# Kernel optimization log

Measured on AMD Instinct MI355X. Metric: run time of the kernel, lower is better.

## Reference

```python
import jax, jax.numpy as jnp
import numpy as np

RPN_BBOX_STD_DEV = np.array([0.1, 0.1, 0.2, 0.2], dtype=np.float32)
PRE_NMS_LIMIT = 6000
PROPOSAL_COUNT = 1000
NMS_THRESHOLD = 0.7
BATCH = 8
NUM_ANCHORS = 261888


def setup_inputs() -> dict:
    key = jax.random.key(0)
    k1, k2, k3, k4 = jax.random.split(key, 4)
    fg = jax.random.uniform(k1, (BATCH, NUM_ANCHORS), dtype=jnp.float32)
    rpn_probs = jnp.stack([1.0 - fg, fg], axis=-1)  # [B, N, 2] (bg, fg)
    rpn_bbox = jax.random.normal(k2, (BATCH, NUM_ANCHORS, 4), dtype=jnp.float32) * 0.5
    # valid normalized anchors: y_min < y_max, x_min < x_max, inside [0, 1]
    mins = jax.random.uniform(k3, (BATCH, NUM_ANCHORS, 2), minval=0.0, maxval=0.85)
    size = jax.random.uniform(k4, (BATCH, NUM_ANCHORS, 2), minval=0.02, maxval=0.15)
    anchors = jnp.concatenate([mins, mins + size], axis=-1)  # [B, N, 4]
    return {"rpn_probs": rpn_probs, "rpn_bbox": rpn_bbox, "anchors": anchors}


def apply_box_deltas(boxes, deltas):
    # boxes: [..., (y1, x1, y2, x2)], deltas: [..., (dy, dx, log(dh), log(dw))]
    h = boxes[..., 2] - boxes[..., 0]
    w = boxes[..., 3] - boxes[..., 1]
    cy = boxes[..., 0] + 0.5 * h + deltas[..., 0] * h
    cx = boxes[..., 1] + 0.5 * w + deltas[..., 1] * w
    h = h * jnp.exp(deltas[..., 2])
    w = w * jnp.exp(deltas[..., 3])
    y1 = cy - 0.5 * h
    x1 = cx - 0.5 * w
    return jnp.stack([y1, x1, y1 + h, x1 + w], axis=-1)


def pairwise_iou(boxes):
    # boxes: [N, 4] -> iou [N, N]
    y1, x1, y2, x2 = boxes[:, 0], boxes[:, 1], boxes[:, 2], boxes[:, 3]
    area = (y2 - y1) * (x2 - x1)
    ih = jnp.maximum(jnp.minimum(y2[:, None], y2[None, :]) - jnp.maximum(y1[:, None], y1[None, :]), 0.0)
    iw = jnp.maximum(jnp.minimum(x2[:, None], x2[None, :]) - jnp.maximum(x1[:, None], x1[None, :]), 0.0)
    inter = ih * iw
    union = area[:, None] + area[None, :] - inter
    return jnp.where(union > 0.0, inter / union, 0.0)


def nms_single(boxes):
    # boxes: [K, 4], already sorted by score descending (top_k sorted=True).
    # Greedy NMS: a box is suppressed if it overlaps (IoU > thresh) a kept,
    # higher-scoring box. Sequential suppression via lax.scan over rows.
    K = boxes.shape[0]
    iou = pairwise_iou(boxes)  # [K, K]
    order = jnp.arange(K)

    def step(keep, i):
        suppress = keep[i] & (iou[i] > NMS_THRESHOLD) & (order > i)
        return keep & ~suppress, None

    keep, _ = jax.lax.scan(step, jnp.ones((K,), dtype=bool), order)
    # gather kept boxes in score order, pad with zeros to PROPOSAL_COUNT
    rank = jnp.cumsum(keep) - 1
    valid = keep & (rank < PROPOSAL_COUNT)
    dest = jnp.where(valid, rank, PROPOSAL_COUNT)  # invalid rows -> scratch row
    out = jnp.zeros((PROPOSAL_COUNT + 1, 4), boxes.dtype).at[dest].set(boxes)
    return out[:PROPOSAL_COUNT]


def reference(rpn_probs, rpn_bbox, anchors):
    scores = rpn_probs[:, :, 1]  # fg prob [B, N]
    deltas = rpn_bbox * jnp.asarray(RPN_BBOX_STD_DEV).reshape(1, 1, 4)
    k = min(PRE_NMS_LIMIT, anchors.shape[1])
    top_scores, idx = jax.lax.top_k(scores, k)  # sorted descending, [B, K]
    deltas_k = jnp.take_along_axis(deltas, idx[..., None], axis=1)   # [B, K, 4]
    anchors_k = jnp.take_along_axis(anchors, idx[..., None], axis=1)  # [B, K, 4]
    boxes = jnp.clip(apply_box_deltas(anchors_k, deltas_k), 0.0, 1.0)
    proposals = jax.vmap(nms_single)(boxes)  # [B, PROPOSAL_COUNT, 4]
    return proposals
```

## Files before the change

### kernel.cpp

```cpp
#include <hip/hip_runtime.h>
#include <hip/hip_bf16.h>

typedef unsigned long long ull;

constexpr int BATCH = 8;
constexpr int NA    = 261888;
constexpr int KSEL  = 6000;
constexpr int PROP  = 1000;
constexpr int CAP   = 8192;
constexpr int NBINS = 8192;
constexpr int HB    = 16;
constexpr int NB    = (KSEL + 63) / 64;
constexpr int NWP   = 94;
constexpr int NBLK  = 94;
constexpr int NBLK2 = 47;

constexpr size_t OFF_CNT   = 0;
constexpr size_t OFF_TSEL  = 512;
constexpr size_t OFF_BOXES = 544;
constexpr size_t OFF_MASK  = 769024;
constexpr size_t OFF_DIAG  = OFF_MASK + 36096000;
constexpr size_t OFF_SUP   = OFF_DIAG + 385024;
constexpr size_t OFF_KEYS  = OFF_MASK;
constexpr size_t OFF_RANK  = OFF_MASK + 524288;
constexpr size_t OFF_HIST  = OFF_MASK + 2097152;

__device__ __forceinline__ int score_bin(float s) {
  int b = (int)(s * (float)NBINS);
  if (b < 0) b = 0;
  if (b > NBINS - 1) b = NBINS - 1;
  return b;
}

__global__ __launch_bounds__(256) void hist_kernel(const float2* __restrict__ probs,
                                                   unsigned int* __restrict__ hist) {
  __shared__ unsigned int lh[NBINS];
  for (int i = threadIdx.x; i < NBINS; i += 256) lh[i] = 0u;
  __syncthreads();
  int b = blockIdx.y;
  const float2* p = probs + (size_t)b * NA;
  for (int a = blockIdx.x * 256 + threadIdx.x; a < NA; a += HB * 256) {
    atomicAdd(&lh[score_bin(p[a].y)], 1u);
  }
  __syncthreads();
  unsigned int* gh = hist + ((size_t)b * HB + blockIdx.x) * NBINS;
  for (int i = threadIdx.x; i < NBINS; i += 256) gh[i] = lh[i];
}

__global__ __launch_bounds__(256) void thresh_kernel(const unsigned int* __restrict__ hist,
                                                     int* __restrict__ tsel) {
  constexpr int GR = NBINS / 256;
  __shared__ unsigned int ch[NBINS];
  __shared__ unsigned int gsum[256];
  int b = blockIdx.x;
  const unsigned int* h = hist + (size_t)b * HB * NBINS;
  for (int bin = threadIdx.x; bin < NBINS; bin += 256) {
    unsigned int s = 0;
    for (int k = 0; k < HB; ++k) s += h[(size_t)k * NBINS + bin];
    ch[bin] = s;
  }
  __syncthreads();
  unsigned int s = 0;
  int g0 = threadIdx.x * GR;
  for (int i = 0; i < GR; ++i) s += ch[g0 + i];
  gsum[threadIdx.x] = s;
  __syncthreads();
  if (threadIdx.x == 0) {
    unsigned int acc = 0;
    int g = 255;
    for (; g > 0; --g) {
      if (acc + gsum[g] >= (unsigned)KSEL) break;
      acc += gsum[g];
    }
    int t = g * GR;
    for (int bin = g * GR + GR - 1; bin >= g * GR; --bin) {
      acc += ch[bin];
      if (acc >= (unsigned)KSEL) { t = bin; break; }
    }
    tsel[b] = t;
  }
}

__global__ __launch_bounds__(256) void compact_kernel(const float2* __restrict__ probs,
                                                      const int* __restrict__ tsel,
                                                      int* __restrict__ cnt,
                                                      ull* __restrict__ keys) {
  __shared__ int lcnt, lbase;
  __shared__ ull lbuf[2048];
  int b = blockIdx.y;
  int t = tsel[b];
  if (threadIdx.x == 0) lcnt = 0;
  __syncthreads();
  const float2* p = probs + (size_t)b * NA;
  for (int a = blockIdx.x * blockDim.x + threadIdx.x; a < NA; a += gridDim.x * blockDim.x) {
    float s = p[a].y;
    if (score_bin(s) >= t) {
      int pos = atomicAdd(&lcnt, 1);
      unsigned int ib = ~__float_as_uint(s);
      lbuf[pos] = ((ull)ib << 32) | (unsigned int)a;
    }
  }
  __syncthreads();
  if (threadIdx.x == 0) lbase = atomicAdd(&cnt[b * 16], lcnt);
  __syncthreads();
  int n = lcnt, base = lbase;
  ull* kb = keys + (size_t)b * CAP;
  for (int i = threadIdx.x; i < n; i += 256) {
    int pos = base + i;
    if (pos < CAP) kb[pos] = lbuf[i];
  }
}

__global__ __launch_bounds__(256) void rank_kernel(const int* __restrict__ cnt,
                                                   const ull* __restrict__ keys,
                                                   unsigned int* __restrict__ rank) {
  int b = blockIdx.z;
  int n = cnt[b * 16];
  if (n > CAP) n = CAP;
  int i = blockIdx.x * 256 + threadIdx.x;
  if (i >= n) return;
  const ull* kb = keys + (size_t)b * CAP;
  ull my = kb[i];
  int n16 = (n + 15) & ~15;
  int nchunks = n16 >> 4;
  int hc = nchunks >> 1;
  int jlo = (blockIdx.y == 0) ? 0 : hc * 16;
  int jhi = (blockIdx.y == 0) ? hc * 16 : n16;
  unsigned int r = 0;
  for (int j = jlo; j < jhi; j += 16) {
#pragma unroll
    for (int t = 0; t < 16; ++t) {
      r += (kb[j + t] < my) ? 1u : 0u;
    }
  }
  if (r) atomicAdd(&rank[(size_t)b * CAP + i], r);
}

__global__ __launch_bounds__(256) void scatter_kernel(const float4* __restrict__ anchors4,
                                                      const float4* __restrict__ bbox4,
                                                      const int* __restrict__ cnt,
                                                      const ull* __restrict__ keys,
                                                      const unsigned int* __restrict__ rank,
                                                      float4* __restrict__ boxes4) {
#pragma clang fp contract(off)
  int b = blockIdx.y;
  int n = cnt[b * 16];
  if (n > CAP) n = CAP;
  int i = blockIdx.x * 256 + threadIdx.x;
  if (i >= n) return;
  unsigned int r = rank[(size_t)b * CAP + i];
  if (r >= (unsigned)KSEL) return;
  int a = (int)(unsigned int)(keys[(size_t)b * CAP + i] & 0xffffffffull);
  float4 anc = anchors4[(size_t)b * NA + a];
  float4 d   = bbox4[(size_t)b * NA + a];
  float h = anc.z - anc.x;
  float w = anc.w - anc.y;
  float dy = d.x * 0.1f, dx = d.y * 0.1f, dh = d.z * 0.2f, dw = d.w * 0.2f;
  float cy = (anc.x + (0.5f * h)) + (dy * h);
  float cx = (anc.y + (0.5f * w)) + (dx * w);
  float h2 = h * expf(dh);
  float w2 = w * expf(dw);
  float y1 = cy - 0.5f * h2;
  float x1 = cx - 0.5f * w2;
  float y2 = y1 + h2;
  float x2 = x1 + w2;
  y1 = fminf(fmaxf(y1, 0.f), 1.f);
  x1 = fminf(fmaxf(x1, 0.f), 1.f);
  y2 = fminf(fmaxf(y2, 0.f), 1.f);
  x2 = fminf(fmaxf(x2, 0.f), 1.f);
  boxes4[(size_t)b * KSEL + r] = make_float4(y1, x1, y2, x2);
}

__global__ __launch_bounds__(256) void mask_kernel(const float4* __restrict__ boxes4,
                                                   ull* __restrict__ mask,
                                                   ull* __restrict__ diagT,
                                                   ull* __restrict__ superT) {
#pragma clang fp contract(off)
  int cx = blockIdx.x, rb2 = blockIdx.y, b = blockIdx.z;
  int w0 = 2 * rb2;
  int cb0 = w0 + 4 * cx;
  if (cb0 >= NWP) return;
  __shared__ float4 colbox[4][64];
  __shared__ float  colca[4][64];
  __shared__ ull wtile[128][5];
  int tid = threadIdx.x, wv = tid >> 6, l = tid & 63;
  int cb = cb0 + wv;
  int rA = rb2 * 128 + l, rB = rA + 64;
  float4 zero = make_float4(0.f, 0.f, 0.f, 0.f);
  float4 boxA = (rA < KSEL) ? boxes4[(size_t)b * KSEL + rA] : zero;
  float4 boxB = (rB < KSEL) ? boxes4[(size_t)b * KSEL + rB] : zero;
  float areaA = (boxA.z - boxA.x) * (boxA.w - boxA.y);
  float areaB = (boxB.z - boxB.x) * (boxB.w - boxB.y);
  int c = cb * 64 + l;
  float4 cload = (cb < NB && c < KSEL) ? boxes4[(size_t)b * KSEL + c] : zero;
  colbox[wv][l] = cload;
  colca[wv][l] = (cload.z - cload.x) * (cload.w - cload.y);
  __syncthreads();
  ull bitsA = 0ull, bitsB = 0ull;
  if (cb < NB) {
#pragma unroll
    for (int u = 0; u < 64; ++u) {
      float4 cbx = colbox[wv][u];
      float ca = colca[wv][u];
      {
        float ih = fmaxf(fminf(boxA.z, cbx.z) - fmaxf(boxA.x, cbx.x), 0.f);
        float iw = fmaxf(fminf(boxA.w, cbx.w) - fmaxf(boxA.y, cbx.y), 0.f);
        float inter = ih * iw;
        float uni = (areaA + ca) - inter;
        float d = fmaf(-0.7f, uni, inter);
        float tt = 6e-7f * uni;
        bool keep;
        if (__builtin_fabsf(d) <= tt) keep = (inter / uni) > 0.7f;
        else keep = d > 0.f;
        if (keep) bitsA |= (1ull << u);
      }
      {
        float ih = fmaxf(fminf(boxB.z, cbx.z) - fmaxf(boxB.x, cbx.x), 0.f);
        float iw = fmaxf(fminf(boxB.w, cbx.w) - fmaxf(boxB.y, cbx.y), 0.f);
        float inter = ih * iw;
        float uni = (areaB + ca) - inter;
        float d = fmaf(-0.7f, uni, inter);
        float tt = 6e-7f * uni;
        bool keep;
        if (__builtin_fabsf(d) <= tt) keep = (inter / uni) > 0.7f;
        else keep = d > 0.f;
        if (keep) bitsB |= (1ull << u);
      }
    }
    if (cb == w0) {
      bitsA &= (l == 63) ? 0ull : (~0ull << (l + 1));
      ull colT = 0ull;
#pragma unroll
      for (int k = 0; k < 64; ++k) {
        ull bk = __ballot(((bitsA >> k) & 1ull) != 0ull);
        if (l == k) colT = bk;
      }
      diagT[((size_t)b * NBLK + w0) * 64 + l] = colT;
    }
    if (cb == w0 + 1) {
      superT[((size_t)b * NBLK + w0) * 64 + l] = bitsA;
      bitsB &= (l == 63) ? 0ull : (~0ull << (l + 1));
      ull colT = 0ull;
#pragma unroll
      for (int k = 0; k < 64; ++k) {
        ull bk = __ballot(((bitsB >> k) & 1ull) != 0ull);
        if (l == k) colT = bk;
      }
      diagT[((size_t)b * NBLK + w0 + 1) * 64 + l] = colT;
    }
    if (cb == w0 + 2) {
      superT[((size_t)b * NBLK + w0 + 1) * 64 + l] = bitsB;
    }
  }
  wtile[l][wv] = bitsA;
  wtile[l + 64][wv] = bitsB;
  __syncthreads();
  int base_row = rb2 * 128;
#pragma unroll
  for (int pass = 0; pass < 2; ++pass) {
    int idx = pass * 256 + tid;
    int rr = idx >> 2, w = idx & 3;
    int row = base_row + rr;
    if (row < KSEL && cb0 + w < NWP)
      mask[((size_t)b * KSEL + row) * NWP + cb0 + w] = wtile[rr][w];
  }
}

__global__ __launch_bounds__(256, 1) void scan_kernel(const float4* __restrict__ boxes4,
                                                      const ull* __restrict__ mask,
                                                      const ull* __restrict__ diagT,
                                                      const ull* __restrict__ superT,
                                                      float4* __restrict__ out4) {
  __shared__ ull ldiagT[NBLK * 64];
  __shared__ ull lsuper[NBLK * 64];
  __shared__ ull S[96];
  __shared__ ull S_urg;
  __shared__ int klist[2][64];
  __shared__ int skeep[1024];
  __shared__ int s_kept, s_done, s_klen[2];
  int b = blockIdx.x;
  int tid = threadIdx.x;
  int lane = tid & 63;
  const ull* mb = mask + (size_t)b * KSEL * NWP;

  const ull* dt = diagT + (size_t)b * NBLK * 64;
  const ull* st = superT + (size_t)b * NBLK * 64;
  for (int i = tid; i < NBLK * 64; i += 256) { ldiagT[i] = dt[i]; lsuper[i] = st[i]; }
  if (tid < 96) S[tid] = 0ull;
  if (tid == 0) { s_kept = 0; s_done = 0; s_klen[0] = 0; s_klen[1] = 0; S_urg = 0ull; }
  __syncthreads();

  for (int n = 0; n < NBLK; ++n) {
    if (tid < 64) {
      ull Sn = S[n] | S_urg;
      int i0 = n * 64;
      ull colT = ldiagT[i0 + lane];
      ull sd = (n + 1 < NBLK) ? lsuper[i0 + lane] : 0ull;
      int nval = KSEL - i0;
      ull valid = (nval >= 64) ? ~0ull : ((1ull << nval) - 1ull);
      ull A = ~Sn & valid;
      ull K = 0ull;
      int kept = s_kept;
      int done = 0;
      while (A) {
        int u = __builtin_ctzll(A);
        ++kept;
        K |= (1ull << u);
        if (kept >= PROP) { done = 1; break; }
        ull sup = __ballot(((colT >> u) & 1ull) != 0ull);
        A &= ~(sup | (1ull << u));
      }
      int klen = __builtin_popcountll(K);
      int kbase = kept - klen;
      if ((K >> lane) & 1ull) {
        int rank = __builtin_popcountll(K & ((1ull << lane) - 1ull));
        skeep[kbase + rank] = i0 + lane;
        klist[n & 1][rank] = i0 + lane;
      }
      int klp = (klen + 7) & ~7;
      if (klen > 0 && lane >= klen && lane < klp)
        klist[n & 1][lane] = i0 + __builtin_ctzll(K);
      unsigned ulo = (unsigned)sd, uhi = (unsigned)(sd >> 32);
      if (!((K >> lane) & 1ull)) { ulo = 0u; uhi = 0u; }
#pragma unroll
      for (int m = 1; m < 64; m <<= 1) {
        ulo |= (unsigned)__shfl_xor((int)ulo, m, 64);
        uhi |= (unsigned)__shfl_xor((int)uhi, m, 64);
      }
      if (lane == 0) {
        s_klen[n & 1] = klen;
        S_urg = (ull)ulo | ((ull)uhi << 32);
        s_kept = kept;
        if (done || n == NBLK - 1) s_done = 1;
      }
    } else {
      int prev = (n & 1) ^ 1;
      int kl = s_klen[prev];
      int w = n + 1 + (tid - 64);
      if (kl > 0 && w < NB) {
        const int* kp = klist[prev];
        ull acc = 0ull;
        int klp = (kl + 7) & ~7;
        for (int ri = 0; ri < klp; ri += 8) {
#pragma unroll
          for (int t2 = 0; t2 < 8; ++t2)
            acc |= mb[(size_t)kp[ri + t2] * NWP + w];
        }
        S[w] |= acc;
      }
    }
    __syncthreads();
    if (s_done) break;
  }

  int fin = s_kept;
  if (fin > PROP) fin = PROP;
  for (int r2 = tid; r2 < PROP; r2 += 256) {
    float4 v = make_float4(0.f, 0.f, 0.f, 0.f);
    if (r2 < fin) v = boxes4[(size_t)b * KSEL + skeep[r2]];
    out4[(size_t)b * PROP + r2] = v;
  }
}

extern "C" void kernel_launch(void* const* d_in, const int* in_sizes, int n_in,
                              void* d_out, int out_size, void* d_ws, size_t ws_size,
                              hipStream_t stream) {
  const float2* probs   = (const float2*)d_in[0];
  const float4* bbox4   = (const float4*)d_in[1];
  const float4* anchors4= (const float4*)d_in[2];
  float4* out4 = (float4*)d_out;
  char* ws = (char*)d_ws;

  int* cnt           = (int*)(ws + OFF_CNT);
  int* tsel          = (int*)(ws + OFF_TSEL);
  float4* boxes4     = (float4*)(ws + OFF_BOXES);
  ull* maskw         = (ull*)(ws + OFF_MASK);
  ull* diagT         = (ull*)(ws + OFF_DIAG);
  ull* superT        = (ull*)(ws + OFF_SUP);
  ull* keys          = (ull*)(ws + OFF_KEYS);
  unsigned int* rank = (unsigned int*)(ws + OFF_RANK);
  unsigned int* hist = (unsigned int*)(ws + OFF_HIST);

  hipMemsetAsync(ws + OFF_CNT, 0, 544, stream);
  hipMemsetAsync(ws + OFF_KEYS, 0xFF, 524288, stream);
  hipMemsetAsync(ws + OFF_RANK, 0, 262144, stream);

  hipLaunchKernelGGL(hist_kernel,    dim3(HB, BATCH),      dim3(256), 0, stream, probs, hist);
  hipLaunchKernelGGL(thresh_kernel,  dim3(BATCH),          dim3(256), 0, stream, hist, tsel);
  hipLaunchKernelGGL(compact_kernel, dim3(128, BATCH),     dim3(256), 0, stream, probs, tsel, cnt, keys);
  hipLaunchKernelGGL(rank_kernel,    dim3(32, 2, BATCH),   dim3(256), 0, stream, cnt, keys, rank);
  hipLaunchKernelGGL(scatter_kernel, dim3(32, BATCH),      dim3(256), 0, stream, anchors4, bbox4, cnt, keys, rank, boxes4);
  hipLaunchKernelGGL(mask_kernel,    dim3(24, NBLK2, BATCH), dim3(256), 0, stream, boxes4, maskw, diagT, superT);
  hipLaunchKernelGGL(scan_kernel,    dim3(BATCH),          dim3(256), 0, stream, boxes4, maskw, diagT, superT, out4);
}
```

Baseline: 347.8 us.

## Restructure IoU mask kernel to broadcast row boxes via readlane and ballot

The mask kernel changes from each lane holding two row boxes and looping over column boxes staged in shared memory to each lane holding one column box. Row box coordinates are broadcast with readlane, and each row's 64-bit mask word is built with a wave ballot. This removes the shared-memory staging, the per-lane bit accumulation and the two-row register state. In exchange, the grid doubles in row blocks, so column boxes are reloaded for every 64-row block and each row-block kernel does half the work.

```diff
diff --git a/kernel.cpp b/kernel.cpp
--- a/kernel.cpp
+++ b/kernel.cpp
@@ -13,7 +13,6 @@
 constexpr int NB    = (KSEL + 63) / 64;
 constexpr int NWP   = 94;
 constexpr int NBLK  = 94;
-constexpr int NBLK2 = 47;
 
 constexpr size_t OFF_CNT   = 0;
 constexpr size_t OFF_TSEL  = 512;
@@ -30,6 +29,10 @@
   if (b < 0) b = 0;
   if (b > NBINS - 1) b = NBINS - 1;
   return b;
+}
+
+__device__ __forceinline__ float bcast(float v, int r) {
+  return __int_as_float(__builtin_amdgcn_readlane(__float_as_int(v), r));
 }
 
 __global__ __launch_bounds__(256) void hist_kernel(const float2* __restrict__ probs,
@@ -176,94 +179,65 @@
                                                    ull* __restrict__ diagT,
                                                    ull* __restrict__ superT) {
 #pragma clang fp contract(off)
-  int cx = blockIdx.x, rb2 = blockIdx.y, b = blockIdx.z;
-  int w0 = 2 * rb2;
-  int cb0 = w0 + 4 * cx;
+  int cx = blockIdx.x, rb = blockIdx.y, b = blockIdx.z;
+  int cb0 = rb + 4 * cx;
   if (cb0 >= NWP) return;
-  __shared__ float4 colbox[4][64];
-  __shared__ float  colca[4][64];
-  __shared__ ull wtile[128][5];
+  __shared__ ull wtile[64][5];
   int tid = threadIdx.x, wv = tid >> 6, l = tid & 63;
   int cb = cb0 + wv;
-  int rA = rb2 * 128 + l, rB = rA + 64;
   float4 zero = make_float4(0.f, 0.f, 0.f, 0.f);
-  float4 boxA = (rA < KSEL) ? boxes4[(size_t)b * KSEL + rA] : zero;
-  float4 boxB = (rB < KSEL) ? boxes4[(size_t)b * KSEL + rB] : zero;
-  float areaA = (boxA.z - boxA.x) * (boxA.w - boxA.y);
-  float areaB = (boxB.z - boxB.x) * (boxB.w - boxB.y);
+  int row = rb * 64 + l;
+  float4 rbox = (row < KSEL) ? boxes4[(size_t)b * KSEL + row] : zero;
+  float rarea = (rbox.z - rbox.x) * (rbox.w - rbox.y);
+  bool vcb = (cb < NB);
   int c = cb * 64 + l;
-  float4 cload = (cb < NB && c < KSEL) ? boxes4[(size_t)b * KSEL + c] : zero;
-  colbox[wv][l] = cload;
-  colca[wv][l] = (cload.z - cload.x) * (cload.w - cload.y);
-  __syncthreads();
-  ull bitsA = 0ull, bitsB = 0ull;
-  if (cb < NB) {
-#pragma unroll
-    for (int u = 0; u < 64; ++u) {
-      float4 cbx = colbox[wv][u];
-      float ca = colca[wv][u];
-      {
-        float ih = fmaxf(fminf(boxA.z, cbx.z) - fmaxf(boxA.x, cbx.x), 0.f);
-        float iw = fmaxf(fminf(boxA.w, cbx.w) - fmaxf(boxA.y, cbx.y), 0.f);
-        float inter = ih * iw;
-        float uni = (areaA + ca) - inter;
-        float d = fmaf(-0.7f, uni, inter);
-        float tt = 6e-7f * uni;
-        bool keep;
-        if (__builtin_fabsf(d) <= tt) keep = (inter / uni) > 0.7f;
-        else keep = d > 0.f;
-        if (keep) bitsA |= (1ull << u);
-      }
-      {
-        float ih = fmaxf(fminf(boxB.z, cbx.z) - fmaxf(boxB.x, cbx.x), 0.f);
-        float iw = fmaxf(fminf(boxB.w, cbx.w) - fmaxf(boxB.y, cbx.y), 0.f);
-        float inter = ih * iw;
-        float uni = (areaB + ca) - inter;
-        float d = fmaf(-0.7f, uni, inter);
-        float tt = 6e-7f * uni;
-        bool keep;
-        if (__builtin_fabsf(d) <= tt) keep = (inter / uni) > 0.7f;
-        else keep = d > 0.f;
-        if (keep) bitsB |= (1ull << u);
-      }
-    }
-    if (cb == w0) {
-      bitsA &= (l == 63) ? 0ull : (~0ull << (l + 1));
+  float4 cbox = (vcb && c < KSEL) ? boxes4[(size_t)b * KSEL + c] : zero;
+  float ca = (cbox.z - cbox.x) * (cbox.w - cbox.y);
+  ull myword = 0ull;
+  if (vcb) {
+    bool isdiag = (cb == rb);
+#pragma unroll
+    for (int r = 0; r < 64; ++r) {
+      float ry1 = bcast(rbox.x, r);
+      float rx1 = bcast(rbox.y, r);
+      float ry2 = bcast(rbox.z, r);
+      float rx2 = bcast(rbox.w, r);
+      float rA  = bcast(rarea,  r);
+      float ih = fmaxf(fminf(ry2, cbox.z) - fmaxf(ry1, cbox.x), 0.f);
+      float iw = fmaxf(fminf(rx2, cbox.w) - fmaxf(rx1, cbox.y), 0.f);
+      float inter = ih * iw;
+      float uni = (rA + ca) - inter;
+      float d = fmaf(-0.7f, uni, inter);
+      float tt = 6e-7f * uni;
+      bool keep;
+      if (__builtin_fabsf(d) <= tt) {
+        keep = (inter / uni) > 0.7f;
+      } else {
+        keep = d > 0.f;
+      }
+      ull bits = __ballot(keep);
+      if (isdiag) bits &= (r == 63) ? 0ull : (~0ull << (r + 1));
+      if (l == r) myword = bits;
+    }
+    if (isdiag) {
       ull colT = 0ull;
 #pragma unroll
       for (int k = 0; k < 64; ++k) {
-        ull bk = __ballot(((bitsA >> k) & 1ull) != 0ull);
+        ull bk = __ballot(((myword >> k) & 1ull) != 0ull);
         if (l == k) colT = bk;
       }
-      diagT[((size_t)b * NBLK + w0) * 64 + l] = colT;
-    }
-    if (cb == w0 + 1) {
-      superT[((size_t)b * NBLK + w0) * 64 + l] = bitsA;
-      bitsB &= (l == 63) ? 0ull : (~0ull << (l + 1));
-      ull colT = 0ull;
-#pragma unroll
-      for (int k = 0; k < 64; ++k) {
-        ull bk = __ballot(((bitsB >> k) & 1ull) != 0ull);
-        if (l == k) colT = bk;
-      }
-      diagT[((size_t)b * NBLK + w0 + 1) * 64 + l] = colT;
-    }
-    if (cb == w0 + 2) {
-      superT[((size_t)b * NBLK + w0 + 1) * 64 + l] = bitsB;
-    }
-  }
-  wtile[l][wv] = bitsA;
-  wtile[l + 64][wv] = bitsB;
-  __syncthreads();
-  int base_row = rb2 * 128;
-#pragma unroll
-  for (int pass = 0; pass < 2; ++pass) {
-    int idx = pass * 256 + tid;
-    int rr = idx >> 2, w = idx & 3;
-    int row = base_row + rr;
-    if (row < KSEL && cb0 + w < NWP)
-      mask[((size_t)b * KSEL + row) * NWP + cb0 + w] = wtile[rr][w];
-  }
+      diagT[((size_t)b * NBLK + rb) * 64 + l] = colT;
+    }
+    if (cb == rb + 1) {
+      superT[((size_t)b * NBLK + rb) * 64 + l] = myword;
+    }
+  }
+  wtile[l][wv] = myword;
+  __syncthreads();
+  int rr = tid >> 2, w = tid & 3;
+  int orow = rb * 64 + rr;
+  if (orow < KSEL && cb0 + w < NWP)
+    mask[((size_t)b * KSEL + orow) * NWP + cb0 + w] = wtile[rr][w];
 }
 
 __global__ __launch_bounds__(256, 1) void scan_kernel(const float4* __restrict__ boxes4,
@@ -390,6 +364,6 @@
   hipLaunchKernelGGL(compact_kernel, dim3(128, BATCH),     dim3(256), 0, stream, probs, tsel, cnt, keys);
   hipLaunchKernelGGL(rank_kernel,    dim3(32, 2, BATCH),   dim3(256), 0, stream, cnt, keys, rank);
   hipLaunchKernelGGL(scatter_kernel, dim3(32, BATCH),      dim3(256), 0, stream, anchors4, bbox4, cnt, keys, rank, boxes4);
-  hipLaunchKernelGGL(mask_kernel,    dim3(24, NBLK2, BATCH), dim3(256), 0, stream, boxes4, maskw, diagT, superT);
+  hipLaunchKernelGGL(mask_kernel,    dim3(24, NBLK, BATCH), dim3(256), 0, stream, boxes4, maskw, diagT, superT);
   hipLaunchKernelGGL(scan_kernel,    dim3(BATCH),          dim3(256), 0, stream, boxes4, maskw, diagT, superT, out4);
 }
```

Result: slower. 403.3 us (+16.0%).

## Fuse rank and scatter kernels and fold workspace memsets into hist kernel

Applied to the files above, without the earlier changes.

Removes the three hipMemsetAsync calls by having hist_kernel zero the counters and fill the key buffer with sentinel values. Merges rank_kernel and scatter_kernel into one kernel, so the rank array and its atomics go away and each thread does the full rank loop itself. This trades two launches and the memsets for a rank pass with half as many blocks, each doing twice the loop length. It relies on hist_kernel's 128 blocks covering exactly the cnt and key regions that need initialising.

```diff
diff --git a/kernel.cpp b/kernel.cpp
--- a/kernel.cpp
+++ b/kernel.cpp
@@ -22,7 +22,6 @@
 constexpr size_t OFF_DIAG  = OFF_MASK + 36096000;
 constexpr size_t OFF_SUP   = OFF_DIAG + 385024;
 constexpr size_t OFF_KEYS  = OFF_MASK;
-constexpr size_t OFF_RANK  = OFF_MASK + 524288;
 constexpr size_t OFF_HIST  = OFF_MASK + 2097152;
 
 __device__ __forceinline__ int score_bin(float s) {
@@ -33,9 +32,17 @@
 }
 
 __global__ __launch_bounds__(256) void hist_kernel(const float2* __restrict__ probs,
-                                                   unsigned int* __restrict__ hist) {
+                                                   unsigned int* __restrict__ hist,
+                                                   int* __restrict__ cnt,
+                                                   ull* __restrict__ keys) {
   __shared__ unsigned int lh[NBINS];
   for (int i = threadIdx.x; i < NBINS; i += 256) lh[i] = 0u;
+  int fb = blockIdx.y * HB + blockIdx.x;
+  if (threadIdx.x == 0) cnt[fb] = 0;
+  {
+    ull* kp = keys + (size_t)fb * 512;
+    for (int i = threadIdx.x; i < 512; i += 256) kp[i] = ~0ull;
+  }
   __syncthreads();
   int b = blockIdx.y;
   const float2* p = probs + (size_t)b * NA;
@@ -111,10 +118,13 @@
   }
 }
 
-__global__ __launch_bounds__(256) void rank_kernel(const int* __restrict__ cnt,
-                                                   const ull* __restrict__ keys,
-                                                   unsigned int* __restrict__ rank) {
-  int b = blockIdx.z;
+__global__ __launch_bounds__(256) void rankscatter_kernel(const float4* __restrict__ anchors4,
+                                                          const float4* __restrict__ bbox4,
+                                                          const int* __restrict__ cnt,
+                                                          const ull* __restrict__ keys,
+                                                          float4* __restrict__ boxes4) {
+#pragma clang fp contract(off)
+  int b = blockIdx.y;
   int n = cnt[b * 16];
   if (n > CAP) n = CAP;
   int i = blockIdx.x * 256 + threadIdx.x;
@@ -122,35 +132,15 @@
   const ull* kb = keys + (size_t)b * CAP;
   ull my = kb[i];
   int n16 = (n + 15) & ~15;
-  int nchunks = n16 >> 4;
-  int hc = nchunks >> 1;
-  int jlo = (blockIdx.y == 0) ? 0 : hc * 16;
-  int jhi = (blockIdx.y == 0) ? hc * 16 : n16;
   unsigned int r = 0;
-  for (int j = jlo; j < jhi; j += 16) {
+  for (int j = 0; j < n16; j += 16) {
 #pragma unroll
     for (int t = 0; t < 16; ++t) {
       r += (kb[j + t] < my) ? 1u : 0u;
     }
   }
-  if (r) atomicAdd(&rank[(size_t)b * CAP + i], r);
-}
-
-__global__ __launch_bounds__(256) void scatter_kernel(const float4* __restrict__ anchors4,
-                                                      const float4* __restrict__ bbox4,
-                                                      const int* __restrict__ cnt,
-                                                      const ull* __restrict__ keys,
-                                                      const unsigned int* __restrict__ rank,
-                                                      float4* __restrict__ boxes4) {
-#pragma clang fp contract(off)
-  int b = blockIdx.y;
-  int n = cnt[b * 16];
-  if (n > CAP) n = CAP;
-  int i = blockIdx.x * 256 + threadIdx.x;
-  if (i >= n) return;
-  unsigned int r = rank[(size_t)b * CAP + i];
   if (r >= (unsigned)KSEL) return;
-  int a = (int)(unsigned int)(keys[(size_t)b * CAP + i] & 0xffffffffull);
+  int a = (int)(unsigned int)(my & 0xffffffffull);
   float4 anc = anchors4[(size_t)b * NA + a];
   float4 d   = bbox4[(size_t)b * NA + a];
   float h = anc.z - anc.x;
@@ -378,18 +368,12 @@
   ull* diagT         = (ull*)(ws + OFF_DIAG);
   ull* superT        = (ull*)(ws + OFF_SUP);
   ull* keys          = (ull*)(ws + OFF_KEYS);
-  unsigned int* rank = (unsigned int*)(ws + OFF_RANK);
   unsigned int* hist = (unsigned int*)(ws + OFF_HIST);
 
-  hipMemsetAsync(ws + OFF_CNT, 0, 544, stream);
-  hipMemsetAsync(ws + OFF_KEYS, 0xFF, 524288, stream);
-  hipMemsetAsync(ws + OFF_RANK, 0, 262144, stream);
-
-  hipLaunchKernelGGL(hist_kernel,    dim3(HB, BATCH),      dim3(256), 0, stream, probs, hist);
-  hipLaunchKernelGGL(thresh_kernel,  dim3(BATCH),          dim3(256), 0, stream, hist, tsel);
-  hipLaunchKernelGGL(compact_kernel, dim3(128, BATCH),     dim3(256), 0, stream, probs, tsel, cnt, keys);
-  hipLaunchKernelGGL(rank_kernel,    dim3(32, 2, BATCH),   dim3(256), 0, stream, cnt, keys, rank);
-  hipLaunchKernelGGL(scatter_kernel, dim3(32, BATCH),      dim3(256), 0, stream, anchors4, bbox4, cnt, keys, rank, boxes4);
-  hipLaunchKernelGGL(mask_kernel,    dim3(24, NBLK2, BATCH), dim3(256), 0, stream, boxes4, maskw, diagT, superT);
-  hipLaunchKernelGGL(scan_kernel,    dim3(BATCH),          dim3(256), 0, stream, boxes4, maskw, diagT, superT, out4);
-}
+  hipLaunchKernelGGL(hist_kernel,        dim3(HB, BATCH),      dim3(256), 0, stream, probs, hist, cnt, keys);
+  hipLaunchKernelGGL(thresh_kernel,      dim3(BATCH),          dim3(256), 0, stream, hist, tsel);
+  hipLaunchKernelGGL(compact_kernel,     dim3(128, BATCH),     dim3(256), 0, stream, probs, tsel, cnt, keys);
+  hipLaunchKernelGGL(rankscatter_kernel, dim3(32, BATCH),      dim3(256), 0, stream, anchors4, bbox4, cnt, keys, boxes4);
+  hipLaunchKernelGGL(mask_kernel,        dim3(24, NBLK2, BATCH), dim3(256), 0, stream, boxes4, maskw, diagT, superT);
+  hipLaunchKernelGGL(scan_kernel,        dim3(BATCH),          dim3(256), 0, stream, boxes4, maskw, diagT, superT, out4);
+}
```

Measured after the change: 391.1 us. 12.5% more time.
